# Optimization experiments

Measured on AMD Instinct MI355X. Metric: run time of the kernel, lower is better.

The kernel has to match this reference:

```python
import jax, jax.numpy as jnp
import numpy as np

NUM_HEADS = 16

def setup_inputs() -> dict:
    key = jax.random.key(0)
    ks = jax.random.split(key, 5)
    d_model = 1024
    x = jax.random.normal(ks[0], (2, 2048, d_model), dtype=jnp.float32)
    # xavier-uniform-like scale for square [d_model, d_model] weights
    lim = float(np.sqrt(6.0 / (d_model + d_model)))
    def w(k):
        return jax.random.uniform(k, (d_model, d_model), dtype=jnp.float32, minval=-lim, maxval=lim)
    return {"x": x, "Wq": w(ks[1]), "Wk": w(ks[2]), "Wv": w(ks[3]), "Wo": w(ks[4])}

def reference(x, Wq, Wk, Wv, Wo):
    B, S, D = x.shape
    H = NUM_HEADS
    dk = D // H
    # project: torch does x @ W.T
    def split_heads(t):
        return t.reshape(B, S, H, dk).transpose(0, 2, 1, 3)  # [B,H,S,dk]
    q = split_heads(x @ Wq.T)
    k = split_heads(x @ Wk.T)
    v = split_heads(x @ Wv.T)
    scores = jnp.einsum('bhqd,bhkd->bhqk', q, k) / jnp.sqrt(jnp.float32(dk))
    causal = jnp.tril(jnp.ones((S, S), dtype=bool))  # True where attended
    scores = jnp.where(causal[None, None], scores, -jnp.inf)
    probs = jax.nn.softmax(scores, axis=-1)
    out = jnp.einsum('bhqk,bhkd->bhqd', probs, v)  # [B,H,S,dk]
    out = out.transpose(0, 2, 1, 3).reshape(B, S, D)
    return out @ Wo.T
```

## Files before the change

### kernel.cpp

```cpp
#include <hip/hip_runtime.h>
#include <stdint.h>

#define BATCH  2
#define SEQ    2048
#define DMODEL 1024
#define NHEADS 16
#define DKH    64
#define MTOT   (BATCH*SEQ)
#define VSTR   (SEQ + 32)

typedef unsigned short u16;
typedef __bf16 bf16x8 __attribute__((ext_vector_type(8)));
typedef float  f32x4  __attribute__((ext_vector_type(4)));

extern "C" __device__ float __ocml_native_exp2_f32(float);

__device__ __forceinline__ u16 f2bf(float f) {
  union { float f; uint32_t u; } v; v.f = f;
  uint32_t u = v.u;
  return (u16)((u + 0x7FFFu + ((u >> 16) & 1u)) >> 16);
}
__device__ __forceinline__ float bf2f(u16 h) {
  union { uint32_t u; float f; } v; v.u = (uint32_t)h << 16; return v.f;
}

__device__ __forceinline__ void gld_lds16(const void* g, void* l) {
  __builtin_amdgcn_global_load_lds(
      (__attribute__((address_space(1))) void*)g,
      (__attribute__((address_space(3))) void*)l, 16, 0, 0);
}

__global__ void cvt_f32_bf16(const float* __restrict__ src, u16* __restrict__ dst) {
  size_t i = ((size_t)blockIdx.x * 256 + threadIdx.x) * 4;
  float4 f = *(const float4*)(src + i);
  ushort4 o;
  o.x = f2bf(f.x); o.y = f2bf(f.y); o.z = f2bf(f.z); o.w = f2bf(f.w);
  *(ushort4*)(dst + i) = o;
}
__global__ void cvt_w(const float* __restrict__ a, const float* __restrict__ b,
                      const float* __restrict__ c, const float* __restrict__ d,
                      u16* __restrict__ dst) {
  const float* srcs[4] = {a, b, c, d};
  const float* s = srcs[blockIdx.y];
  size_t i = ((size_t)blockIdx.x * 256 + threadIdx.x) * 4;
  float4 f = *(const float4*)(s + i);
  ushort4 o;
  o.x = f2bf(f.x); o.y = f2bf(f.y); o.z = f2bf(f.z); o.w = f2bf(f.w);
  *(ushort4*)(dst + (size_t)blockIdx.y * (DMODEL*DMODEL) + i) = o;
}

__global__ __launch_bounds__(256, 3) void gemm_qkv(
    const u16* __restrict__ xb, const u16* __restrict__ wq,
    const u16* __restrict__ wk, const u16* __restrict__ wv,
    u16* __restrict__ q, u16* __restrict__ k, u16* __restrict__ v, float qscale) {
  __shared__ __align__(16) u16 lA[128 * 64];
  __shared__ __align__(16) u16 lB[3][64 * 64];

  const int tid  = threadIdx.x;
  const int lane = tid & 63;
  const int lrow = lane & 15;
  const int quad = lane >> 4;
  const int wave = tid >> 6;
  const int wm   = (wave & 1) * 64;
  const int wn   = (wave >> 1) * 32;
  const int sx   = lrow & 7;
  const int m0 = blockIdx.x * 128, n0 = blockIdx.y * 64;
  const u16* Ws[3] = {wq, wk, wv};

  f32x4 acc[3][4][2] = {};

  for (int k0 = 0; k0 < DMODEL; k0 += 64) {
    #pragma unroll
    for (int r = 0; r < 4; ++r) {
      int off  = r * 4096 + tid * 16;
      int row  = off >> 7;
      int c16  = (off >> 4) & 7;
      int colb = (c16 ^ (row & 7)) << 4;
      gld_lds16((const char*)xb + ((size_t)(m0 + row) * DMODEL + k0) * 2 + colb,
                (char*)lA + off);
    }
    #pragma unroll
    for (int z = 0; z < 3; ++z)
      #pragma unroll
      for (int r = 0; r < 2; ++r) {
        int off  = r * 4096 + tid * 16;
        int row  = off >> 7;
        int c16  = (off >> 4) & 7;
        int colb = (c16 ^ (row & 7)) << 4;
        gld_lds16((const char*)Ws[z] + ((size_t)(n0 + row) * DMODEL + k0) * 2 + colb,
                  (char*)&lB[z][0] + off);
      }
    __syncthreads();
    #pragma unroll
    for (int ks = 0; ks < 2; ++ks) {
      const int ro = ((((ks << 2) | quad) ^ sx) << 3);
      bf16x8 a[4], b[3][2];
      #pragma unroll
      for (int i = 0; i < 4; ++i)
        a[i] = *(const bf16x8*)(lA + (wm + i*16 + lrow) * 64 + ro);
      #pragma unroll
      for (int z = 0; z < 3; ++z)
        #pragma unroll
        for (int j = 0; j < 2; ++j)
          b[z][j] = *(const bf16x8*)(&lB[z][0] + (wn + j*16 + lrow) * 64 + ro);
      #pragma unroll
      for (int z = 0; z < 3; ++z)
        #pragma unroll
        for (int i = 0; i < 4; ++i)
          #pragma unroll
          for (int j = 0; j < 2; ++j)
            acc[z][i][j] = __builtin_amdgcn_mfma_f32_16x16x32_bf16(a[i], b[z][j], acc[z][i][j], 0, 0, 0);
    }
    __syncthreads();
  }

  const int rb = quad * 4, cb = lrow;
  const int h  = blockIdx.y;
  u16* outs[3] = {q, k, v};
  #pragma unroll
  for (int z = 0; z < 3; ++z) {
    u16* out = outs[z];
    if (z == 2) {
      #pragma unroll
      for (int i = 0; i < 4; ++i)
        #pragma unroll
        for (int j = 0; j < 2; ++j) {
          int row0 = m0 + wm + i*16 + rb;
          int d_   = wn + j*16 + cb;
          int b_ = row0 >> 11, s0 = row0 & 2047;
          ushort4 pk;
          pk.x = f2bf(acc[z][i][j][0]); pk.y = f2bf(acc[z][i][j][1]);
          pk.z = f2bf(acc[z][i][j][2]); pk.w = f2bf(acc[z][i][j][3]);
          *(ushort4*)&out[((size_t)(b_*NHEADS + h) * DKH + d_) * VSTR + s0] = pk;
        }
    } else {
      const float scale = (z == 0) ? qscale : 1.0f;
      #pragma unroll
      for (int i = 0; i < 4; ++i)
        #pragma unroll
        for (int j = 0; j < 2; ++j)
          #pragma unroll
          for (int r = 0; r < 4; ++r) {
            int row = m0 + wm + i*16 + rb + r;
            int d_  = wn + j*16 + cb;
            int b_ = row >> 11, s_ = row & 2047;
            out[(((size_t)(b_*NHEADS + h) * SEQ + s_) << 6) + d_] =
                f2bf(acc[z][i][j][r] * scale);
          }
    }
  }
}

__device__ __forceinline__ void gemm_core64(const u16* A, const u16* W,
                                            int m0, int n0, f32x4 acc[4][2],
                                            u16* lA, u16* lB) {
  const int tid  = threadIdx.x;
  const int lane = tid & 63;
  const int lrow = lane & 15;
  const int quad = lane >> 4;
  const int wave = tid >> 6;
  const int wm   = (wave & 1) * 64;
  const int wn   = (wave >> 1) * 32;
  const int sx   = lrow & 7;

  for (int k0 = 0; k0 < DMODEL; k0 += 64) {
    #pragma unroll
    for (int r = 0; r < 4; ++r) {
      int off  = r * 4096 + tid * 16;
      int row  = off >> 7;
      int c16  = (off >> 4) & 7;
      int colb = (c16 ^ (row & 7)) << 4;
      gld_lds16((const char*)A + ((size_t)(m0 + row) * DMODEL + k0) * 2 + colb,
                (char*)lA + off);
    }
    #pragma unroll
    for (int r = 0; r < 2; ++r) {
      int off  = r * 4096 + tid * 16;
      int row  = off >> 7;
      int c16  = (off >> 4) & 7;
      int colb = (c16 ^ (row & 7)) << 4;
      gld_lds16((const char*)W + ((size_t)(n0 + row) * DMODEL + k0) * 2 + colb,
                (char*)lB + off);
    }
    __syncthreads();
    #pragma unroll
    for (int ks = 0; ks < 2; ++ks) {
      bf16x8 a[4], b[2];
      const int ro = ((((ks << 2) | quad) ^ sx) << 3);
      #pragma unroll
      for (int i = 0; i < 4; ++i)
        a[i] = *(const bf16x8*)(lA + (wm + i*16 + lrow) * 64 + ro);
      #pragma unroll
      for (int j = 0; j < 2; ++j)
        b[j] = *(const bf16x8*)(lB + (wn + j*16 + lrow) * 64 + ro);
      #pragma unroll
      for (int i = 0; i < 4; ++i)
        #pragma unroll
        for (int j = 0; j < 2; ++j)
          acc[i][j] = __builtin_amdgcn_mfma_f32_16x16x32_bf16(a[i], b[j], acc[i][j], 0, 0, 0);
    }
    __syncthreads();
  }
}

__global__ __launch_bounds__(256, 3) void gemm_out(
    const u16* __restrict__ ab, const u16* __restrict__ wo, float* __restrict__ out) {
  __shared__ __align__(16) u16 lA[128 * 64];
  __shared__ __align__(16) u16 lB[64 * 64];
  const int m0 = blockIdx.x * 128, n0 = blockIdx.y * 64;
  f32x4 acc[4][2] = {};
  gemm_core64(ab, wo, m0, n0, acc, lA, lB);

  const int lane = threadIdx.x & 63;
  const int wave = threadIdx.x >> 6;
  const int wm = (wave & 1) * 64, wn = (wave >> 1) * 32;
  const int rb = (lane >> 4) * 4, cb = lane & 15;
  #pragma unroll
  for (int i = 0; i < 4; ++i)
    #pragma unroll
    for (int j = 0; j < 2; ++j)
      #pragma unroll
      for (int r = 0; r < 4; ++r)
        out[(size_t)(m0 + wm + i*16 + rb + r) * DMODEL + (n0 + wn + j*16 + cb)]
            = acc[i][j][r];
}

#define PSTR 68
__device__ const uint8_t JT[80] = {
  124,125,126,127, 120,121,122, 116,117,118, 112,113,114, 108,109,110,
  104,105,106, 100,101,102, 96,97,98, 92,93,94, 88,89, 84,85, 80,81,
  76,77, 72,73, 68,69, 64,65, 60,61, 56, 52, 48, 44, 40, 36, 32, 28,
  123,90,57,24, 119,86,53,20, 115,82,49,16, 111,78,45,12,
  107,74,41,8, 103,70,37,4, 99,66,33,0
};

__global__ __launch_bounds__(64, 2) void attn(
    const u16* __restrict__ Q, const u16* __restrict__ K,
    const u16* __restrict__ V, u16* __restrict__ O,
    u16* __restrict__ po, float* __restrict__ pl) {
  __shared__ __align__(16) u16 Ps[4][16 * PSTR];

  const int lane = threadIdx.x & 63;
  const int lrow = lane & 15;
  const int quad = lane >> 4;
  const int kq   = quad * 8;

  const int g  = blockIdx.x >> 5;
  const int bh = blockIdx.x & 31;
  const int e  = JT[g];
  const int p  = e >> 2, c = e & 3;
  const int lo = c * 8;
  const int hi = (p + 1 < lo + 8) ? p + 1 : lo + 8;

  const u16* Qg = Q + (size_t)bh * SEQ * DKH;
  const u16* Kg = K + (size_t)bh * SEQ * DKH;
  const u16* Vg = V + (size_t)bh * DKH * VSTR;

  bf16x8 aq[4][2];
  #pragma unroll
  for (int i = 0; i < 4; ++i)
    #pragma unroll
    for (int ks = 0; ks < 2; ++ks)
      aq[i][ks] = *(const bf16x8*)(Qg + (size_t)(64*p + 16*i + lrow) * DKH + ks*32 + kq);

  f32x4 o_acc[4][4] = {};
  float l_acc[4][4] = {};

  const u16* kbase = Kg + (size_t)lrow * DKH + kq;
  const u16* vbase = Vg + (size_t)lrow * VSTR + kq;

  for (int t = lo; t < hi; ++t) {
    bf16x8 kf[2][4], vf[2][4];
    #pragma unroll
    for (int ks = 0; ks < 2; ++ks)
      #pragma unroll
      for (int j = 0; j < 4; ++j) {
        kf[ks][j] = *(const bf16x8*)(kbase + (size_t)t*64*DKH + j*16*DKH + ks*32);
        vf[ks][j] = *(const bf16x8*)(vbase + t*64 + (size_t)j*16*VSTR + ks*32);
      }
    const bool mk = (t == p);

    #pragma unroll
    for (int i = 0; i < 4; ++i) {
      f32x4 s_acc[4] = {};
      #pragma unroll
      for (int ks = 0; ks < 2; ++ks)
        #pragma unroll
        for (int j = 0; j < 4; ++j)
          s_acc[j] = __builtin_amdgcn_mfma_f32_16x16x32_bf16(aq[i][ks], kf[ks][j], s_acc[j], 0, 0, 0);

      if (mk) {
        const int qloc = 16*i + quad*4;
        #pragma unroll
        for (int j = 0; j < 4; ++j) {
          int kloc = j*16 + lrow;
          #pragma unroll
          for (int r = 0; r < 4; ++r)
            if (kloc > qloc + r) s_acc[j][r] = -1e30f;
        }
      }

      #pragma unroll
      for (int j = 0; j < 4; ++j)
        #pragma unroll
        for (int r = 0; r < 4; ++r) {
          float pv = __ocml_native_exp2_f32(s_acc[j][r]);
          l_acc[i][r] += pv;
          union { float f; uint32_t u; } cv; cv.f = pv;
          Ps[i][(quad*4 + r) * PSTR + j*16 + lrow] = (u16)(cv.u >> 16);
        }

      #pragma unroll
      for (int ks = 0; ks < 2; ++ks) {
        bf16x8 ap = *(const bf16x8*)(&Ps[i][lrow * PSTR + ks*32 + kq]);
        #pragma unroll
        for (int j = 0; j < 4; ++j)
          o_acc[i][j] = __builtin_amdgcn_mfma_f32_16x16x32_bf16(ap, vf[ks][j], o_acc[i][j], 0, 0, 0);
      }
    }
  }

  float lr[4][4];
  #pragma unroll
  for (int i = 0; i < 4; ++i)
    #pragma unroll
    for (int r = 0; r < 4; ++r) {
      float sm = l_acc[i][r];
      #pragma unroll
      for (int d = 1; d < 16; d <<= 1) sm += __shfl_xor(sm, d, 64);
      lr[i][r] = sm;
    }

  if (p <= 7) {
    const int h = bh & 15, b_ = bh >> 4;
    #pragma unroll
    for (int i = 0; i < 4; ++i)
      #pragma unroll
      for (int j = 0; j < 4; ++j)
        #pragma unroll
        for (int r = 0; r < 4; ++r) {
          int sg = 64*p + 16*i + quad*4 + r;
          O[(size_t)(b_ * SEQ + sg) * DMODEL + h * DKH + j*16 + lrow]
              = f2bf(o_acc[i][j][r] / lr[i][r]);
        }
  } else {
    const int base = (p < 16) ? (p - 8) * 2
                   : (p < 24) ? 16 + (p - 16) * 3
                   :            40 + (p - 24) * 4;
    const int slot = (base + c) * 32 + bh;
    #pragma unroll
    for (int i = 0; i < 4; ++i) {
      #pragma unroll
      for (int j = 0; j < 4; ++j) {
        ushort4 pk;
        pk.x = f2bf(o_acc[i][j][0]); pk.y = f2bf(o_acc[i][j][1]);
        pk.z = f2bf(o_acc[i][j][2]); pk.w = f2bf(o_acc[i][j][3]);
        *(ushort4*)&po[(size_t)slot * 4096 + (j*16 + lrow) * 64 + 16*i + quad*4] = pk;
      }
      if (lrow == 0)
        #pragma unroll
        for (int r = 0; r < 4; ++r)
          pl[slot * 64 + 16*i + quad*4 + r] = lr[i][r];
    }
  }
}

__global__ __launch_bounds__(256) void combine(
    const u16* __restrict__ po, const float* __restrict__ pl, u16* __restrict__ ab) {
  __shared__ u16 Ls[64][68];
  const int b  = blockIdx.x;
  const int p  = 8 + (b >> 5);
  const int bh = b & 31;
  const int t  = threadIdx.x;
  const int col = t >> 2;
  const int r0  = (t & 3) * 16;
  const int base = (p < 16) ? (p - 8) * 2
                 : (p < 24) ? 16 + (p - 16) * 3
                 :            40 + (p - 24) * 4;
  const int nc   = (p < 16) ? 2 : (p < 24) ? 3 : 4;

  float acc[16], lsum[16];
  const size_t s0 = (size_t)(base * 32 + bh);
  const u16*   q0 = po + s0 * 4096 + col * 64 + r0;
  const float* l0 = pl + s0 * 64 + r0;
  #pragma unroll
  for (int q4 = 0; q4 < 4; ++q4) {
    ushort4 a  = *(const ushort4*)(q0 + q4 * 4);
    ushort4 c2 = *(const ushort4*)(q0 + (size_t)32 * 4096 + q4 * 4);
    acc[q4*4+0] = bf2f(a.x) + bf2f(c2.x);
    acc[q4*4+1] = bf2f(a.y) + bf2f(c2.y);
    acc[q4*4+2] = bf2f(a.z) + bf2f(c2.z);
    acc[q4*4+3] = bf2f(a.w) + bf2f(c2.w);
    float4 f = *(const float4*)(l0 + q4 * 4);
    float4 g = *(const float4*)(l0 + 32 * 64 + q4 * 4);
    lsum[q4*4+0] = f.x + g.x; lsum[q4*4+1] = f.y + g.y;
    lsum[q4*4+2] = f.z + g.z; lsum[q4*4+3] = f.w + g.w;
  }
  if (nc >= 3) {
    #pragma unroll
    for (int q4 = 0; q4 < 4; ++q4) {
      ushort4 a = *(const ushort4*)(q0 + (size_t)64 * 4096 + q4 * 4);
      acc[q4*4+0] += bf2f(a.x); acc[q4*4+1] += bf2f(a.y);
      acc[q4*4+2] += bf2f(a.z); acc[q4*4+3] += bf2f(a.w);
      float4 f = *(const float4*)(l0 + 64 * 64 + q4 * 4);
      lsum[q4*4+0] += f.x; lsum[q4*4+1] += f.y;
      lsum[q4*4+2] += f.z; lsum[q4*4+3] += f.w;
    }
  }
  if (nc == 4) {
    #pragma unroll
    for (int q4 = 0; q4 < 4; ++q4) {
      ushort4 a = *(const ushort4*)(q0 + (size_t)96 * 4096 + q4 * 4);
      acc[q4*4+0] += bf2f(a.x); acc[q4*4+1] += bf2f(a.y);
      acc[q4*4+2] += bf2f(a.z); acc[q4*4+3] += bf2f(a.w);
      float4 f = *(const float4*)(l0 + 96 * 64 + q4 * 4);
      lsum[q4*4+0] += f.x; lsum[q4*4+1] += f.y;
      lsum[q4*4+2] += f.z; lsum[q4*4+3] += f.w;
    }
  }
  #pragma unroll
  for (int q = 0; q < 16; ++q)
    Ls[r0 + q][col] = f2bf(acc[q] / lsum[q]);
  __syncthreads();

  const int row = t >> 2;
  const int c0  = (t & 3) * 16;
  const int b_ = bh >> 4, h = bh & 15;
  u16* dst = ab + (size_t)(b_ * SEQ + 64 * p + row) * DMODEL + h * DKH + c0;
  #pragma unroll
  for (int q = 0; q < 16; q += 4)
    *(ushort4*)(dst + q) = *(const ushort4*)&Ls[row][c0 + q];
}

extern "C" void kernel_launch(void* const* d_in, const int* in_sizes, int n_in,
                              void* d_out, int out_size, void* d_ws, size_t ws_size,
                              hipStream_t stream) {
  const float* x  = (const float*)d_in[0];
  const float* Wq = (const float*)d_in[1];
  const float* Wk = (const float*)d_in[2];
  const float* Wv = (const float*)d_in[3];
  const float* Wo = (const float*)d_in[4];
  float* out = (float*)d_out;

  u16* xb  = (u16*)d_ws;
  u16* wqb = xb  + (size_t)MTOT * DMODEL;
  u16* wkb = wqb + (size_t)DMODEL * DMODEL;
  u16* wvb = wkb + (size_t)DMODEL * DMODEL;
  u16* wob = wvb + (size_t)DMODEL * DMODEL;
  u16* qb  = wob + (size_t)DMODEL * DMODEL;
  u16* kb  = qb  + (size_t)MTOT * DMODEL;
  u16* vb  = kb  + (size_t)MTOT * DMODEL;
  u16* ab  = vb  + (size_t)BATCH * NHEADS * DKH * VSTR;
  u16* po  = ab  + (size_t)MTOT * DMODEL;
  float* pl = (float*)(po + (size_t)2304 * 4096);

  cvt_f32_bf16<<<MTOT * DMODEL / 1024, 256, 0, stream>>>(x, xb);
  cvt_w<<<dim3(DMODEL * DMODEL / 1024, 4), 256, 0, stream>>>(Wq, Wk, Wv, Wo, wqb);

  const float qscale = 0.125f * 1.44269504088896340736f;
  gemm_qkv<<<dim3(32, 16), 256, 0, stream>>>(
      xb, wqb, wkb, wvb, qb, kb, vb, qscale);

  attn<<<2560, 64, 0, stream>>>(qb, kb, vb, ab, po, pl);
  combine<<<768, 256, 0, stream>>>(po, pl, ab);

  gemm_out<<<dim3(32, 16), 256, 0, stream>>>(ab, wob, out);
}
```

Baseline: 170.9 us.

## Keep attention probabilities in registers via transposed QK MFMA and permlane swap

Swaps the operand order of the QK^T MFMA so each lane holds score values along the key dimension. The probabilities are then packed to bf16 with v_cvt_pk_bf16_f32 and rearranged with v_permlane16_swap instead of a round trip through LDS. The V fragment loading is permuted to match, and the row-sum reduction changes to match the transposed layout. This removes LDS writes and reads plus their implicit waits from the inner loop. In exchange it relies on getting the lane permutation exactly right and uses gfx950-specific instructions.

```diff
diff --git a/kernel.cpp b/kernel.cpp
--- a/kernel.cpp
+++ b/kernel.cpp
@@ -28,6 +28,15 @@
   __builtin_amdgcn_global_load_lds(
       (__attribute__((address_space(1))) void*)g,
       (__attribute__((address_space(3))) void*)l, 16, 0, 0);
+}
+
+__device__ __forceinline__ uint32_t cvtpk(float lo, float hi) {
+  uint32_t r;
+  asm("v_cvt_pk_bf16_f32 %0, %1, %2" : "=v"(r) : "v"(lo), "v"(hi));
+  return r;
+}
+__device__ __forceinline__ void pl16swap(uint32_t& a, uint32_t& b) {
+  asm volatile("v_permlane16_swap_b32 %0, %1" : "+v"(a), "+v"(b));
 }
 
 __global__ void cvt_f32_bf16(const float* __restrict__ src, u16* __restrict__ dst) {
@@ -238,12 +247,11 @@
     const u16* __restrict__ Q, const u16* __restrict__ K,
     const u16* __restrict__ V, u16* __restrict__ O,
     u16* __restrict__ po, float* __restrict__ pl) {
-  __shared__ __align__(16) u16 Ps[4][16 * PSTR];
-
   const int lane = threadIdx.x & 63;
   const int lrow = lane & 15;
   const int quad = lane >> 4;
   const int kq   = quad * 8;
+  const int vkq  = ((((quad & 1) << 1) | (quad >> 1)) << 3);
 
   const int g  = blockIdx.x >> 5;
   const int bh = blockIdx.x & 31;
@@ -264,10 +272,10 @@
       aq[i][ks] = *(const bf16x8*)(Qg + (size_t)(64*p + 16*i + lrow) * DKH + ks*32 + kq);
 
   f32x4 o_acc[4][4] = {};
-  float l_acc[4][4] = {};
+  float l_acc[4] = {};
 
   const u16* kbase = Kg + (size_t)lrow * DKH + kq;
-  const u16* vbase = Vg + (size_t)lrow * VSTR + kq;
+  const u16* vbase = Vg + (size_t)lrow * VSTR + vkq;
 
   for (int t = lo; t < hi; ++t) {
     bf16x8 kf[2][4], vf[2][4];
@@ -287,49 +295,60 @@
       for (int ks = 0; ks < 2; ++ks)
         #pragma unroll
         for (int j = 0; j < 4; ++j)
-          s_acc[j] = __builtin_amdgcn_mfma_f32_16x16x32_bf16(aq[i][ks], kf[ks][j], s_acc[j], 0, 0, 0);
+          s_acc[j] = __builtin_amdgcn_mfma_f32_16x16x32_bf16(kf[ks][j], aq[i][ks], s_acc[j], 0, 0, 0);
 
       if (mk) {
-        const int qloc = 16*i + quad*4;
+        const int qloc = 16*i + lrow;
         #pragma unroll
         for (int j = 0; j < 4; ++j) {
-          int kloc = j*16 + lrow;
+          int kl = j*16 + quad*4;
           #pragma unroll
           for (int r = 0; r < 4; ++r)
-            if (kloc > qloc + r) s_acc[j][r] = -1e30f;
+            if (kl + r > qloc) s_acc[j][r] = -1e30f;
         }
       }
 
+      uint32_t w[4][2];
+      float ls = 0.f;
+      #pragma unroll
+      for (int j = 0; j < 4; ++j) {
+        float p0 = __ocml_native_exp2_f32(s_acc[j][0]);
+        float p1 = __ocml_native_exp2_f32(s_acc[j][1]);
+        float p2 = __ocml_native_exp2_f32(s_acc[j][2]);
+        float p3 = __ocml_native_exp2_f32(s_acc[j][3]);
+        ls += (p0 + p1) + (p2 + p3);
+        w[j][0] = cvtpk(p0, p1);
+        w[j][1] = cvtpk(p2, p3);
+      }
+      l_acc[i] += ls;
+
+      pl16swap(w[0][0], w[1][0]);
+      pl16swap(w[0][1], w[1][1]);
+      pl16swap(w[2][0], w[3][0]);
+      pl16swap(w[2][1], w[3][1]);
+      union { uint32_t u[4]; bf16x8 v; } g0, g1;
+      g0.u[0] = w[0][0]; g0.u[1] = w[0][1]; g0.u[2] = w[1][0]; g0.u[3] = w[1][1];
+      g1.u[0] = w[2][0]; g1.u[1] = w[2][1]; g1.u[2] = w[3][0]; g1.u[3] = w[3][1];
+
       #pragma unroll
       for (int j = 0; j < 4; ++j)
-        #pragma unroll
-        for (int r = 0; r < 4; ++r) {
-          float pv = __ocml_native_exp2_f32(s_acc[j][r]);
-          l_acc[i][r] += pv;
-          union { float f; uint32_t u; } cv; cv.f = pv;
-          Ps[i][(quad*4 + r) * PSTR + j*16 + lrow] = (u16)(cv.u >> 16);
-        }
-
-      #pragma unroll
-      for (int ks = 0; ks < 2; ++ks) {
-        bf16x8 ap = *(const bf16x8*)(&Ps[i][lrow * PSTR + ks*32 + kq]);
-        #pragma unroll
-        for (int j = 0; j < 4; ++j)
-          o_acc[i][j] = __builtin_amdgcn_mfma_f32_16x16x32_bf16(ap, vf[ks][j], o_acc[i][j], 0, 0, 0);
-      }
+        o_acc[i][j] = __builtin_amdgcn_mfma_f32_16x16x32_bf16(g0.v, vf[0][j], o_acc[i][j], 0, 0, 0);
+      #pragma unroll
+      for (int j = 0; j < 4; ++j)
+        o_acc[i][j] = __builtin_amdgcn_mfma_f32_16x16x32_bf16(g1.v, vf[1][j], o_acc[i][j], 0, 0, 0);
     }
   }
 
   float lr[4][4];
   #pragma unroll
-  for (int i = 0; i < 4; ++i)
-    #pragma unroll
-    for (int r = 0; r < 4; ++r) {
-      float sm = l_acc[i][r];
-      #pragma unroll
-      for (int d = 1; d < 16; d <<= 1) sm += __shfl_xor(sm, d, 64);
-      lr[i][r] = sm;
-    }
+  for (int i = 0; i < 4; ++i) {
+    float s = l_acc[i];
+    s += __shfl_xor(s, 16, 64);
+    s += __shfl_xor(s, 32, 64);
+    #pragma unroll
+    for (int r = 0; r < 4; ++r)
+      lr[i][r] = __shfl(s, quad*4 + r, 16);
+  }
 
   if (p <= 7) {
     const int h = bh & 15, b_ = bh >> 4;
```

Measured after the change: 169.1 us. About the same (-1.0%).
